# Optimization experiments

Hardware: AMD Instinct MI355X
Metric: run time of the kernel (lower is better)

## Reference

```python
import jax, jax.numpy as jnp
import numpy as np

HEADS = 8
DIM_HEAD = 64
SCALE = 10.0
EPS = 1e-12  # F.normalize eps


def setup_inputs() -> dict:
    key = jax.random.key(0)
    k1, k2, k3, k4 = jax.random.split(key, 4)
    dim, hidden = 256, HEADS * DIM_HEAD
    x = jax.random.normal(k1, (8, dim, 32, 32), dtype=jnp.float32)
    w_qkv = jax.random.normal(k2, (3 * hidden, dim), dtype=jnp.float32) * (1.0 / np.sqrt(dim))
    w_out = jax.random.normal(k3, (dim, hidden), dtype=jnp.float32) * (1.0 / np.sqrt(hidden))
    b_out = jax.random.normal(k4, (dim,), dtype=jnp.float32) * 0.01
    return {"x": x, "w_qkv": w_qkv, "w_out": w_out, "b_out": b_out}


def _l2norm_last(t):
    # matches F.normalize(t, dim=-1): t / max(||t||_2, eps)
    n = jnp.sqrt(jnp.sum(t * t, axis=-1, keepdims=True))
    return t / jnp.maximum(n, EPS)


def reference(x, w_qkv, w_out, b_out):
    b, c, hh, ww = x.shape
    n = hh * ww
    # 1x1 conv == channel matmul
    qkv = jnp.einsum('bcxy,oc->boxy', x, w_qkv)  # (b, 3*hidden, h, w)
    q, k, v = jnp.split(qkv, 3, axis=1)
    # 'b (h c) x y -> b h c (x y)'
    to_heads = lambda t: t.reshape(b, HEADS, DIM_HEAD, n)
    q, k, v = to_heads(q), to_heads(k), to_heads(v)
    # NOTE: l2norm over the LAST axis = spatial token axis n (faithful to source)
    q = _l2norm_last(q)
    k = _l2norm_last(k)
    sim = jnp.einsum('bhdi,bhdj->bhij', q, k) * SCALE  # (b, h, n, n)
    attn = jax.nn.softmax(sim, axis=-1)
    out = jnp.einsum('bhij,bhdj->bhid', attn, v)  # (b, h, n, d)
    # 'b h (x y) d -> b (h d) x y'
    out = out.transpose(0, 1, 3, 2).reshape(b, HEADS * DIM_HEAD, hh, ww)
    return jnp.einsum('bcxy,oc->boxy', out, w_out) + b_out[None, :, None, None]
```

## Files before the change

kernel.cpp:

```cpp
#include <hip/hip_runtime.h>
#include <math.h>

#define NHEADS 8
#define DHEAD  64
#define HIDDEN 512
#define CIN    256
#define NTOK   1024
#define QK_SCALE 10.0f
#define LOG2E 1.44269504088896f
#define MSHIFT 10.5f
#define MBIAS  (-MSHIFT * LOG2E)

typedef __bf16 bf16x8 __attribute__((ext_vector_type(8)));
typedef float  f32x4  __attribute__((ext_vector_type(4)));
typedef unsigned short u16x8 __attribute__((ext_vector_type(8)));
typedef unsigned short u16x4 __attribute__((ext_vector_type(4)));

__device__ inline unsigned short f2bf(float f) {
    unsigned u = __builtin_bit_cast(unsigned, f);
    u = (u + 0x7FFFu + ((u >> 16) & 1u)) >> 16;
    return (unsigned short)u;
}

__device__ inline bf16x8 cvt8(const float* p) {
    float4 a = *(const float4*)p;
    float4 b = *(const float4*)(p + 4);
    u16x8 t;
    t[0] = f2bf(a.x); t[1] = f2bf(a.y); t[2] = f2bf(a.z); t[3] = f2bf(a.w);
    t[4] = f2bf(b.x); t[5] = f2bf(b.y); t[6] = f2bf(b.z); t[7] = f2bf(b.w);
    return __builtin_bit_cast(bf16x8, t);
}

__global__ __launch_bounds__(256)
void cvt_x_kernel(const float* __restrict__ x, unsigned short* __restrict__ xt) {
    const int b  = blockIdx.z;
    const int c0 = blockIdx.y * 64;
    const int n0 = blockIdx.x * 64;
    const float* src = x + ((size_t)b * CIN + c0) * NTOK + n0;
    unsigned short* dst = xt + ((size_t)b * NTOK + n0) * CIN + c0;

    __shared__ float T[64][65];
    const int t = threadIdx.x;
    {
        const int nq = t & 15, cg = t >> 4;
        #pragma unroll
        for (int rr = 0; rr < 4; ++rr) {
            const int c = cg + rr * 16;
            float4 v = *(const float4*)(src + (size_t)c * NTOK + nq * 4);
            T[c][nq * 4 + 0] = v.x;
            T[c][nq * 4 + 1] = v.y;
            T[c][nq * 4 + 2] = v.z;
            T[c][nq * 4 + 3] = v.w;
        }
    }
    __syncthreads();
    {
        const int n = t >> 2, cq = t & 3;
        alignas(16) unsigned short tmp[16];
        #pragma unroll
        for (int e = 0; e < 16; ++e)
            tmp[e] = f2bf(T[cq * 16 + e][n]);
        *(uint4*)(dst + (size_t)n * CIN + cq * 16)     = *(uint4*)&tmp[0];
        *(uint4*)(dst + (size_t)n * CIN + cq * 16 + 8) = *(uint4*)&tmp[8];
    }
}

__global__ __launch_bounds__(256)
void cvt_w_kernel(const float* __restrict__ wq, const float* __restrict__ wo,
                  unsigned short* __restrict__ wqb, unsigned short* __restrict__ wob) {
    const size_t i = ((size_t)blockIdx.x * 256 + threadIdx.x) * 8;
    if (i < (size_t)1536 * 256) {
        *(bf16x8*)(wqb + i) = cvt8(wq + i);
    } else {
        const size_t j = i - (size_t)1536 * 256;
        *(bf16x8*)(wob + j) = cvt8(wo + j);
    }
}

__global__ __launch_bounds__(256)
void gemm1_kernel(const unsigned short* __restrict__ wqb,
                  const unsigned short* __restrict__ xt,
                  float* __restrict__ qt,
                  unsigned short* __restrict__ vb,
                  float* __restrict__ ss) {
    const int b  = blockIdx.z;
    const int bm = blockIdx.y * 128;
    const int bn = blockIdx.x * 128;
    const int wave = threadIdx.x >> 6, lane = threadIdx.x & 63;
    const int lo = lane & 15, hi = lane >> 4;
    const int wm = bm + (wave >> 1) * 64;
    const int wn = bn + (wave & 1) * 64;

    const unsigned short* Ab = wqb + (size_t)(wm + lo) * CIN + hi * 8;
    const unsigned short* Bb = xt + ((size_t)b * NTOK + wn + lo) * CIN + hi * 8;

    f32x4 acc[4][4];
    #pragma unroll
    for (int mi = 0; mi < 4; ++mi)
        #pragma unroll
        for (int ni = 0; ni < 4; ++ni) acc[mi][ni] = (f32x4){0.f, 0.f, 0.f, 0.f};

    for (int k0 = 0; k0 < CIN; k0 += 32) {
        bf16x8 a[4], bf[4];
        #pragma unroll
        for (int mi = 0; mi < 4; ++mi) a[mi]  = *(const bf16x8*)(Ab + (size_t)mi * 16 * CIN + k0);
        #pragma unroll
        for (int ni = 0; ni < 4; ++ni) bf[ni] = *(const bf16x8*)(Bb + (size_t)ni * 16 * CIN + k0);
        #pragma unroll
        for (int mi = 0; mi < 4; ++mi)
            #pragma unroll
            for (int ni = 0; ni < 4; ++ni)
                acc[mi][ni] = __builtin_amdgcn_mfma_f32_16x16x32_bf16(a[mi], bf[ni], acc[mi][ni], 0, 0, 0);
    }

    __shared__ unsigned short VL[4][32][72];

    if (bm < 1024) {
        const int isK = (wm >= 512) ? 1 : 0;
        const int ch0 = wm & 511;
        const int head = ch0 >> 6;
        float* dst = qt + (((size_t)isK * 64 + b * 8 + head) * NTOK) * DHEAD;
        #pragma unroll
        for (int mi = 0; mi < 4; ++mi) {
            const int d = mi * 16 + hi * 4;
            #pragma unroll
            for (int ni = 0; ni < 4; ++ni) {
                const int n = wn + ni * 16 + lo;
                *(f32x4*)(dst + (size_t)n * DHEAD + d) = acc[mi][ni];
            }
        }
        float p[4][4];
        #pragma unroll
        for (int mi = 0; mi < 4; ++mi)
            #pragma unroll
            for (int r = 0; r < 4; ++r) {
                float s = 0.f;
                #pragma unroll
                for (int ni = 0; ni < 4; ++ni) s += acc[mi][ni][r] * acc[mi][ni][r];
                p[mi][r] = s;
            }
        #pragma unroll
        for (int off = 1; off < 16; off <<= 1)
            #pragma unroll
            for (int mi = 0; mi < 4; ++mi)
                #pragma unroll
                for (int r = 0; r < 4; ++r)
                    p[mi][r] += __shfl_xor(p[mi][r], off, 64);
        if (lo == 0) {
            #pragma unroll
            for (int mi = 0; mi < 4; ++mi)
                #pragma unroll
                for (int r = 0; r < 4; ++r)
                    atomicAdd(&ss[(size_t)b * 1024 + isK * 512 + ch0 + mi * 16 + hi * 4 + r], p[mi][r]);
        }
    } else {
        const int ch0 = wm - 1024;
        #pragma unroll
        for (int half = 0; half < 2; ++half) {
            #pragma unroll
            for (int mm = 0; mm < 2; ++mm) {
                const int mi = half * 2 + mm;
                #pragma unroll
                for (int ni = 0; ni < 4; ++ni)
                    #pragma unroll
                    for (int r = 0; r < 4; ++r)
                        VL[wave][mm * 16 + hi * 4 + r][ni * 16 + lo] = f2bf(acc[mi][ni][r]);
            }
            #pragma unroll
            for (int i = 0; i < 4; ++i) {
                const int flat = i * 64 + lane;
                const int row = flat >> 3, c = flat & 7;
                uint4 v = *(uint4*)&VL[wave][row][c * 8];
                const int ch = ch0 + half * 32 + row;
                *(uint4*)(vb + ((size_t)b * HIDDEN + ch) * NTOK + wn + c * 8) = v;
            }
        }
    }
}

__global__ __launch_bounds__(256)
void scale_cvt_kernel(const float* __restrict__ qt, const float* __restrict__ ss,
                      unsigned short* __restrict__ qs, unsigned short* __restrict__ ks) {
    const size_t idx = ((size_t)blockIdx.x * 256 + threadIdx.x) * 8;
    const size_t half = (size_t)64 * NTOK * DHEAD;
    const int isK = idx >= half;
    const size_t rem = idx - (size_t)isK * half;
    const int bh = (int)(rem >> 16);
    const int d0 = (int)(rem & 63);
    const int b  = bh >> 3;
    const int ch = isK * 512 + (bh & 7) * 64 + d0;
    const float scl = isK ? 1.0f : QK_SCALE;

    const float* ip = qt + idx;
    float4 v0 = *(const float4*)ip;
    float4 v1 = *(const float4*)(ip + 4);
    float4 q0 = *(const float4*)(ss + (size_t)b * 1024 + ch);
    float4 q1 = *(const float4*)(ss + (size_t)b * 1024 + ch + 4);
    float4 s0, s1;
    s0.x = 1.0f / fmaxf(sqrtf(q0.x), 1e-12f); s0.y = 1.0f / fmaxf(sqrtf(q0.y), 1e-12f);
    s0.z = 1.0f / fmaxf(sqrtf(q0.z), 1e-12f); s0.w = 1.0f / fmaxf(sqrtf(q0.w), 1e-12f);
    s1.x = 1.0f / fmaxf(sqrtf(q1.x), 1e-12f); s1.y = 1.0f / fmaxf(sqrtf(q1.y), 1e-12f);
    s1.z = 1.0f / fmaxf(sqrtf(q1.z), 1e-12f); s1.w = 1.0f / fmaxf(sqrtf(q1.w), 1e-12f);
    u16x8 t;
    t[0] = f2bf(v0.x * s0.x * scl); t[1] = f2bf(v0.y * s0.y * scl);
    t[2] = f2bf(v0.z * s0.z * scl); t[3] = f2bf(v0.w * s0.w * scl);
    t[4] = f2bf(v1.x * s1.x * scl); t[5] = f2bf(v1.y * s1.y * scl);
    t[6] = f2bf(v1.z * s1.z * scl); t[7] = f2bf(v1.w * s1.w * scl);
    *(u16x8*)((isK ? ks : qs) + rem) = t;
}

__global__ __launch_bounds__(256)
void attn_mfma_kernel(const unsigned short* __restrict__ qs,
                      const unsigned short* __restrict__ ks,
                      const unsigned short* __restrict__ vb,
                      float* __restrict__ po, float* __restrict__ pml) {
    const int hw = blockIdx.x;
    const int virt = (hw & 7) * 128 + (hw >> 3);
    const int bh = virt >> 4;
    const int sub = virt & 15;
    const int it = sub & 7;
    const int js = sub >> 3;
    const int b = bh >> 3, h = bh & 7;

    const int lane = threadIdx.x & 63;
    const int wave = threadIdx.x >> 6;
    const int lo = lane & 15;
    const int hi = lane >> 4;
    const int iw = it * 128 + wave * 32;

    const unsigned short* qbh = qs + (size_t)bh * NTOK * DHEAD;
    const unsigned short* kbh = ks + (size_t)bh * NTOK * DHEAD;
    const unsigned short* vbh = vb + ((size_t)b * HIDDEN + h * DHEAD) * NTOK;

    __shared__ unsigned short Plds[4][2048];
    __shared__ float Tlds[4][16][68];
    char* pbase = (char*)&Plds[wave][0];

    bf16x8 aQ[2][2];
    #pragma unroll
    for (int f = 0; f < 2; ++f) {
        const unsigned short* qp = qbh + (size_t)(iw + f * 16 + lo) * DHEAD + hi * 8;
        aQ[f][0] = *(const bf16x8*)qp;
        aQ[f][1] = *(const bf16x8*)(qp + 32);
    }

    float lsum[2][4];
    #pragma unroll
    for (int f = 0; f < 2; ++f)
        #pragma unroll
        for (int r = 0; r < 4; ++r) lsum[f][r] = 0.0f;
    f32x4 acc[2][4];
    #pragma unroll
    for (int f = 0; f < 2; ++f)
        #pragma unroll
        for (int ds = 0; ds < 4; ++ds) acc[f][ds] = (f32x4){0.f, 0.f, 0.f, 0.f};

    for (int jt = 0; jt < 8; ++jt) {
        const int j0 = js * 512 + jt * 64;

        bf16x8 bV[4][2];
        #pragma unroll
        for (int ds = 0; ds < 4; ++ds) {
            const unsigned short* vp = vbh + (size_t)(ds * 16 + lo) * NTOK + j0 + hi * 8;
            bV[ds][0] = *(const bf16x8*)vp;
            bV[ds][1] = *(const bf16x8*)(vp + 32);
        }

        bf16x8 bK[4][2];
        #pragma unroll
        for (int jj = 0; jj < 4; ++jj) {
            const unsigned short* kp = kbh + (size_t)(j0 + jj * 16 + lo) * DHEAD + hi * 8;
            bK[jj][0] = *(const bf16x8*)kp;
            bK[jj][1] = *(const bf16x8*)(kp + 32);
        }

        f32x4 s[2][4];
        __builtin_amdgcn_s_setprio(1);
        #pragma unroll
        for (int jj = 0; jj < 4; ++jj)
            #pragma unroll
            for (int f = 0; f < 2; ++f) {
                f32x4 c = (f32x4){0.f, 0.f, 0.f, 0.f};
                c = __builtin_amdgcn_mfma_f32_16x16x32_bf16(aQ[f][0], bK[jj][0], c, 0, 0, 0);
                c = __builtin_amdgcn_mfma_f32_16x16x32_bf16(aQ[f][1], bK[jj][1], c, 0, 0, 0);
                s[f][jj] = c;
            }
        __builtin_amdgcn_s_setprio(0);

        #pragma unroll
        for (int f = 0; f < 2; ++f)
            #pragma unroll
            for (int jj = 0; jj < 4; ++jj)
                #pragma unroll
                for (int r = 0; r < 4; ++r) {
                    const float p = __builtin_amdgcn_exp2f(fmaf(s[f][jj][r], LOG2E, MBIAS));
                    lsum[f][r] += p;
                    const int row = f * 16 + hi * 4 + r;
                    const int byte = (row * 128 + (jj * 16 + lo) * 2) ^ ((row & 7) << 4);
                    *(unsigned short*)(pbase + byte) = f2bf(p);
                }

        bf16x8 aP[2][2];
        #pragma unroll
        for (int f = 0; f < 2; ++f) {
            const int row = f * 16 + lo;
            const int swz = (lo & 7) << 4;
            aP[f][0] = *(const bf16x8*)(pbase + ((row * 128 + hi * 16) ^ swz));
            aP[f][1] = *(const bf16x8*)(pbase + ((row * 128 + 64 + hi * 16) ^ swz));
        }
        __builtin_amdgcn_s_setprio(1);
        #pragma unroll
        for (int ds = 0; ds < 4; ++ds)
            #pragma unroll
            for (int f = 0; f < 2; ++f) {
                acc[f][ds] = __builtin_amdgcn_mfma_f32_16x16x32_bf16(aP[f][0], bV[ds][0], acc[f][ds], 0, 0, 0);
                acc[f][ds] = __builtin_amdgcn_mfma_f32_16x16x32_bf16(aP[f][1], bV[ds][1], acc[f][ds], 0, 0, 0);
            }
        __builtin_amdgcn_s_setprio(0);
    }

    #pragma unroll
    for (int off = 1; off < 16; off <<= 1)
        #pragma unroll
        for (int f = 0; f < 2; ++f)
            #pragma unroll
            for (int r = 0; r < 4; ++r)
                lsum[f][r] += __shfl_xor(lsum[f][r], off, 64);

    float* pob = po + ((size_t)(js * 64 + bh) * NTOK + iw) * DHEAD;
    #pragma unroll
    for (int f = 0; f < 2; ++f) {
        #pragma unroll
        for (int ds = 0; ds < 4; ++ds)
            #pragma unroll
            for (int r = 0; r < 4; ++r)
                Tlds[wave][hi * 4 + r][ds * 16 + lo] = acc[f][ds][r];
        #pragma unroll
        for (int pass = 0; pass < 4; ++pass) {
            const int flat = pass * 64 + lane;
            const int row = flat >> 4, dq = flat & 15;
            float4 v = *(float4*)&Tlds[wave][row][dq * 4];
            *(float4*)(pob + (size_t)(f * 16 + row) * DHEAD + dq * 4) = v;
        }
        if (lo == 0) {
            #pragma unroll
            for (int r = 0; r < 4; ++r) {
                const int row = iw + f * 16 + hi * 4 + r;
                pml[(size_t)(js * 64 + bh) * NTOK + row] = lsum[f][r];
            }
        }
    }
}

__global__ __launch_bounds__(256)
void combine_kernel(const float* __restrict__ po, const float* __restrict__ pml,
                    unsigned short* __restrict__ attn_t) {
    const size_t fl = ((size_t)blockIdx.x * 256 + threadIdx.x) * 4;
    const int bh  = (int)(fl >> 16);
    const int rem = (int)(fl & 65535);
    const int row = rem >> 6;
    const int d   = rem & 63;
    const int b = bh >> 3, h = bh & 7;
    const size_t SS = (size_t)64 * NTOK * DHEAD;

    const float l1 = pml[(size_t)bh * NTOK + row];
    const float l2 = pml[(size_t)(64 + bh) * NTOK + row];
    const float inv = 1.0f / (l1 + l2);

    const float4 o1 = *(const float4*)(po + fl);
    const float4 o2 = *(const float4*)(po + SS + fl);
    u16x4 r;
    r[0] = f2bf((o1.x + o2.x) * inv);
    r[1] = f2bf((o1.y + o2.y) * inv);
    r[2] = f2bf((o1.z + o2.z) * inv);
    r[3] = f2bf((o1.w + o2.w) * inv);
    *(u16x4*)(attn_t + ((size_t)b * NTOK + row) * HIDDEN + h * DHEAD + d) = r;
}

__global__ __launch_bounds__(128)
void gemm2_kernel(const unsigned short* __restrict__ wob,
                  const unsigned short* __restrict__ attn_t,
                  const float* __restrict__ b_out,
                  float* __restrict__ out) {
    const int b  = blockIdx.z;
    const int bm = blockIdx.y * 64;
    const int bn = blockIdx.x * 128;
    const int wave = threadIdx.x >> 6, lane = threadIdx.x & 63;
    const int lo = lane & 15, hi = lane >> 4;
    const int wn = bn + wave * 64;

    const unsigned short* Ab = wob + (size_t)(bm + lo) * HIDDEN + hi * 8;
    const unsigned short* Bb = attn_t + ((size_t)b * NTOK + wn + lo) * HIDDEN + hi * 8;

    f32x4 acc[4][4];
    #pragma unroll
    for (int mi = 0; mi < 4; ++mi)
        #pragma unroll
        for (int ni = 0; ni < 4; ++ni) acc[mi][ni] = (f32x4){0.f, 0.f, 0.f, 0.f};

    for (int k0 = 0; k0 < HIDDEN; k0 += 32) {
        bf16x8 a[4], bf[4];
        #pragma unroll
        for (int mi = 0; mi < 4; ++mi) a[mi]  = *(const bf16x8*)(Ab + (size_t)mi * 16 * HIDDEN + k0);
        #pragma unroll
        for (int ni = 0; ni < 4; ++ni) bf[ni] = *(const bf16x8*)(Bb + (size_t)ni * 16 * HIDDEN + k0);
        #pragma unroll
        for (int mi = 0; mi < 4; ++mi)
            #pragma unroll
            for (int ni = 0; ni < 4; ++ni)
                acc[mi][ni] = __builtin_amdgcn_mfma_f32_16x16x32_bf16(a[mi], bf[ni], acc[mi][ni], 0, 0, 0);
    }

    __shared__ float OL[2][32][69];
    #pragma unroll
    for (int half = 0; half < 2; ++half) {
        #pragma unroll
        for (int mm = 0; mm < 2; ++mm) {
            const int mi = half * 2 + mm;
            #pragma unroll
            for (int ni = 0; ni < 4; ++ni)
                #pragma unroll
                for (int r = 0; r < 4; ++r)
                    OL[wave][mm * 16 + hi * 4 + r][ni * 16 + lo] = acc[mi][ni][r];
        }
        #pragma unroll
        for (int i = 0; i < 8; ++i) {
            const int flat = i * 64 + lane;
            const int row = flat >> 4, c = flat & 15;
            float4 v = *(float4*)&OL[wave][row][c * 4];
            const int m = bm + half * 32 + row;
            const float bb = b_out[m];
            v.x += bb; v.y += bb; v.z += bb; v.w += bb;
            *(float4*)(out + ((size_t)b * CIN + m) * NTOK + wn + c * 4) = v;
        }
    }
}

extern "C" void kernel_launch(void* const* d_in, const int* in_sizes, int n_in,
                              void* d_out, int out_size, void* d_ws, size_t ws_size,
                              hipStream_t stream) {
    const float* x     = (const float*)d_in[0];
    const float* w_qkv = (const float*)d_in[1];
    const float* w_out = (const float*)d_in[2];
    const float* b_out = (const float*)d_in[3];
    float* out = (float*)d_out;

    char* ws = (char*)d_ws;
    unsigned short* xt  = (unsigned short*)(ws);
    unsigned short* wqb = (unsigned short*)(ws + 4194304);
    unsigned short* wob = (unsigned short*)(ws + 4980736);
    float*          ss  = (float*)(ws + 5242880);
    unsigned short* qs  = (unsigned short*)(ws + 5308416);
    unsigned short* ks  = (unsigned short*)(ws + 13697024);
    unsigned short* vb  = (unsigned short*)(ws + 22085632);
    float*          qt  = (float*)(ws + 30474240);
    float*          po  = (float*)(ws + 30474240);
    unsigned short* attn_t = (unsigned short*)(ws + 5308416);
    float*          pml = (float*)(ws + 64028672);

    hipMemsetAsync(ss, 0, 8 * 1024 * sizeof(float), stream);

    cvt_x_kernel<<<dim3(16, 4, 8), 256, 0, stream>>>(x, xt);
    cvt_w_kernel<<<256, 256, 0, stream>>>(w_qkv, w_out, wqb, wob);

    gemm1_kernel<<<dim3(8, 12, 8), 256, 0, stream>>>(wqb, xt, qt, vb, ss);

    scale_cvt_kernel<<<4096, 256, 0, stream>>>(qt, ss, qs, ks);

    attn_mfma_kernel<<<1024, 256, 0, stream>>>(qs, ks, vb, po, pml);

    combine_kernel<<<4096, 256, 0, stream>>>(po, pml, attn_t);

    gemm2_kernel<<<dim3(8, 4, 8), 128, 0, stream>>>(wob, attn_t, b_out, out);
}
```

Measured before the change: 203.1 us.

## Keep softmax probabilities in registers via transposed MFMA, store partials as bf16

Swaps the operand order of the QK^T MFMA so the score tile comes out laid out to be reused directly as the B operand of the PV MFMA. V is loaded in matching 4-element chunks, and the probabilities are packed with v_cvt_pk_bf16_f32, which removes the LDS round trip for P. The partial output buffer becomes bf16 and the LDS transpose before the output store is dropped, which halves partial-output traffic read by the combine kernel. Blocks shrink to 2 waves with twice the grid. Storing partials in bf16 costs some accuracy before the final normalisation.

```diff
diff --git a/kernel.cpp b/kernel.cpp
--- a/kernel.cpp
+++ b/kernel.cpp
@@ -12,7 +12,9 @@
 #define MBIAS  (-MSHIFT * LOG2E)
 
 typedef __bf16 bf16x8 __attribute__((ext_vector_type(8)));
+typedef __bf16 bf16x4 __attribute__((ext_vector_type(4)));
 typedef float  f32x4  __attribute__((ext_vector_type(4)));
+typedef unsigned u32x4 __attribute__((ext_vector_type(4)));
 typedef unsigned short u16x8 __attribute__((ext_vector_type(8)));
 typedef unsigned short u16x4 __attribute__((ext_vector_type(4)));
 
@@ -20,6 +22,16 @@
     unsigned u = __builtin_bit_cast(unsigned, f);
     u = (u + 0x7FFFu + ((u >> 16) & 1u)) >> 16;
     return (unsigned short)u;
+}
+
+__device__ inline unsigned cvtpk(float a, float b) {
+    unsigned w;
+    asm("v_cvt_pk_bf16_f32 %0, %1, %2" : "=v"(w) : "v"(a), "v"(b));
+    return w;
+}
+
+__device__ inline float bf2f(unsigned short u) {
+    return __builtin_bit_cast(float, (unsigned)u << 16);
 }
 
 __device__ inline bf16x8 cvt8(const float* p) {
@@ -209,32 +221,28 @@
     *(u16x8*)((isK ? ks : qs) + rem) = t;
 }
 
-__global__ __launch_bounds__(256)
+__global__ __launch_bounds__(128)
 void attn_mfma_kernel(const unsigned short* __restrict__ qs,
                       const unsigned short* __restrict__ ks,
                       const unsigned short* __restrict__ vb,
-                      float* __restrict__ po, float* __restrict__ pml) {
+                      unsigned short* __restrict__ po, float* __restrict__ pml) {
     const int hw = blockIdx.x;
-    const int virt = (hw & 7) * 128 + (hw >> 3);
-    const int bh = virt >> 4;
-    const int sub = virt & 15;
-    const int it = sub & 7;
-    const int js = sub >> 3;
+    const int virt = (hw & 7) * 256 + (hw >> 3);
+    const int bh  = virt >> 5;
+    const int sub = virt & 31;
+    const int it  = sub & 15;
+    const int js  = sub >> 4;
     const int b = bh >> 3, h = bh & 7;
 
     const int lane = threadIdx.x & 63;
     const int wave = threadIdx.x >> 6;
     const int lo = lane & 15;
     const int hi = lane >> 4;
-    const int iw = it * 128 + wave * 32;
+    const int iw = it * 64 + wave * 32;
 
     const unsigned short* qbh = qs + (size_t)bh * NTOK * DHEAD;
     const unsigned short* kbh = ks + (size_t)bh * NTOK * DHEAD;
     const unsigned short* vbh = vb + ((size_t)b * HIDDEN + h * DHEAD) * NTOK;
-
-    __shared__ unsigned short Plds[4][2048];
-    __shared__ float Tlds[4][16][68];
-    char* pbase = (char*)&Plds[wave][0];
 
     bf16x8 aQ[2][2];
     #pragma unroll
@@ -244,11 +252,7 @@
         aQ[f][1] = *(const bf16x8*)(qp + 32);
     }
 
-    float lsum[2][4];
-    #pragma unroll
-    for (int f = 0; f < 2; ++f)
-        #pragma unroll
-        for (int r = 0; r < 4; ++r) lsum[f][r] = 0.0f;
+    float lsum[2] = {0.0f, 0.0f};
     f32x4 acc[2][4];
     #pragma unroll
     for (int f = 0; f < 2; ++f)
@@ -258,12 +262,13 @@
     for (int jt = 0; jt < 8; ++jt) {
         const int j0 = js * 512 + jt * 64;
 
-        bf16x8 bV[4][2];
+        bf16x4 bV[4][4];
         #pragma unroll
         for (int ds = 0; ds < 4; ++ds) {
-            const unsigned short* vp = vbh + (size_t)(ds * 16 + lo) * NTOK + j0 + hi * 8;
-            bV[ds][0] = *(const bf16x8*)vp;
-            bV[ds][1] = *(const bf16x8*)(vp + 32);
+            const unsigned short* vp = vbh + (size_t)(ds * 16 + lo) * NTOK + j0 + hi * 4;
+            #pragma unroll
+            for (int u = 0; u < 4; ++u)
+                bV[ds][u] = *(const bf16x4*)(vp + u * 16);
         }
 
         bf16x8 bK[4][2];
@@ -281,79 +286,71 @@
             #pragma unroll
             for (int f = 0; f < 2; ++f) {
                 f32x4 c = (f32x4){0.f, 0.f, 0.f, 0.f};
-                c = __builtin_amdgcn_mfma_f32_16x16x32_bf16(aQ[f][0], bK[jj][0], c, 0, 0, 0);
-                c = __builtin_amdgcn_mfma_f32_16x16x32_bf16(aQ[f][1], bK[jj][1], c, 0, 0, 0);
+                c = __builtin_amdgcn_mfma_f32_16x16x32_bf16(bK[jj][0], aQ[f][0], c, 0, 0, 0);
+                c = __builtin_amdgcn_mfma_f32_16x16x32_bf16(bK[jj][1], aQ[f][1], c, 0, 0, 0);
                 s[f][jj] = c;
             }
         __builtin_amdgcn_s_setprio(0);
 
-        #pragma unroll
-        for (int f = 0; f < 2; ++f)
+        unsigned pw[2][2][4];
+        #pragma unroll
+        for (int f = 0; f < 2; ++f) {
             #pragma unroll
             for (int jj = 0; jj < 4; ++jj)
                 #pragma unroll
                 for (int r = 0; r < 4; ++r) {
                     const float p = __builtin_amdgcn_exp2f(fmaf(s[f][jj][r], LOG2E, MBIAS));
-                    lsum[f][r] += p;
-                    const int row = f * 16 + hi * 4 + r;
-                    const int byte = (row * 128 + (jj * 16 + lo) * 2) ^ ((row & 7) << 4);
-                    *(unsigned short*)(pbase + byte) = f2bf(p);
+                    s[f][jj][r] = p;
+                    lsum[f] += p;
                 }
-
-        bf16x8 aP[2][2];
-        #pragma unroll
-        for (int f = 0; f < 2; ++f) {
-            const int row = f * 16 + lo;
-            const int swz = (lo & 7) << 4;
-            aP[f][0] = *(const bf16x8*)(pbase + ((row * 128 + hi * 16) ^ swz));
-            aP[f][1] = *(const bf16x8*)(pbase + ((row * 128 + 64 + hi * 16) ^ swz));
-        }
+            #pragma unroll
+            for (int t = 0; t < 2; ++t) {
+                pw[f][t][0] = cvtpk(s[f][2 * t][0],     s[f][2 * t][1]);
+                pw[f][t][1] = cvtpk(s[f][2 * t][2],     s[f][2 * t][3]);
+                pw[f][t][2] = cvtpk(s[f][2 * t + 1][0], s[f][2 * t + 1][1]);
+                pw[f][t][3] = cvtpk(s[f][2 * t + 1][2], s[f][2 * t + 1][3]);
+            }
+        }
+
         __builtin_amdgcn_s_setprio(1);
         #pragma unroll
         for (int ds = 0; ds < 4; ++ds)
             #pragma unroll
-            for (int f = 0; f < 2; ++f) {
-                acc[f][ds] = __builtin_amdgcn_mfma_f32_16x16x32_bf16(aP[f][0], bV[ds][0], acc[f][ds], 0, 0, 0);
-                acc[f][ds] = __builtin_amdgcn_mfma_f32_16x16x32_bf16(aP[f][1], bV[ds][1], acc[f][ds], 0, 0, 0);
-            }
+            for (int f = 0; f < 2; ++f)
+                #pragma unroll
+                for (int t = 0; t < 2; ++t) {
+                    const bf16x8 av = __builtin_shufflevector(
+                        bV[ds][2 * t], bV[ds][2 * t + 1], 0, 1, 2, 3, 4, 5, 6, 7);
+                    const bf16x8 bp = __builtin_bit_cast(bf16x8,
+                        (u32x4){pw[f][t][0], pw[f][t][1], pw[f][t][2], pw[f][t][3]});
+                    acc[f][ds] = __builtin_amdgcn_mfma_f32_16x16x32_bf16(av, bp, acc[f][ds], 0, 0, 0);
+                }
         __builtin_amdgcn_s_setprio(0);
     }
 
     #pragma unroll
-    for (int off = 1; off < 16; off <<= 1)
-        #pragma unroll
-        for (int f = 0; f < 2; ++f)
-            #pragma unroll
-            for (int r = 0; r < 4; ++r)
-                lsum[f][r] += __shfl_xor(lsum[f][r], off, 64);
-
-    float* pob = po + ((size_t)(js * 64 + bh) * NTOK + iw) * DHEAD;
-    #pragma unroll
     for (int f = 0; f < 2; ++f) {
-        #pragma unroll
-        for (int ds = 0; ds < 4; ++ds)
-            #pragma unroll
-            for (int r = 0; r < 4; ++r)
-                Tlds[wave][hi * 4 + r][ds * 16 + lo] = acc[f][ds][r];
-        #pragma unroll
-        for (int pass = 0; pass < 4; ++pass) {
-            const int flat = pass * 64 + lane;
-            const int row = flat >> 4, dq = flat & 15;
-            float4 v = *(float4*)&Tlds[wave][row][dq * 4];
-            *(float4*)(pob + (size_t)(f * 16 + row) * DHEAD + dq * 4) = v;
-        }
-        if (lo == 0) {
-            #pragma unroll
-            for (int r = 0; r < 4; ++r) {
-                const int row = iw + f * 16 + hi * 4 + r;
-                pml[(size_t)(js * 64 + bh) * NTOK + row] = lsum[f][r];
-            }
-        }
+        lsum[f] += __shfl_xor(lsum[f], 16, 64);
+        lsum[f] += __shfl_xor(lsum[f], 32, 64);
+    }
+
+    unsigned short* pob = po + ((size_t)(js * 64 + bh) * NTOK + iw) * DHEAD;
+    #pragma unroll
+    for (int f = 0; f < 2; ++f) {
+        #pragma unroll
+        for (int ds = 0; ds < 4; ++ds) {
+            uint2 w;
+            w.x = cvtpk(acc[f][ds][0], acc[f][ds][1]);
+            w.y = cvtpk(acc[f][ds][2], acc[f][ds][3]);
+            *(uint2*)(pob + (size_t)(f * 16 + lo) * DHEAD + ds * 16 + hi * 4) = w;
+        }
+        if (hi == 0)
+            pml[(size_t)(js * 64 + bh) * NTOK + iw + f * 16 + lo] = lsum[f];
     }
 }
 
 __global__ __launch_bounds__(256)
-void combine_kernel(const float* __restrict__ po, const float* __restrict__ pml,
+void combine_kernel(const unsigned short* __restrict__ po, const float* __restrict__ pml,
                     unsigned short* __restrict__ attn_t) {
     const size_t fl = ((size_t)blockIdx.x * 256 + threadIdx.x) * 4;
     const int bh  = (int)(fl >> 16);
@@ -367,13 +364,12 @@
     const float l2 = pml[(size_t)(64 + bh) * NTOK + row];
     const float inv = 1.0f / (l1 + l2);
 
-    const float4 o1 = *(const float4*)(po + fl);
-    const float4 o2 = *(const float4*)(po + SS + fl);
+    const u16x4 o1 = *(const u16x4*)(po + fl);
+    const u16x4 o2 = *(const u16x4*)(po + SS + fl);
     u16x4 r;
-    r[0] = f2bf((o1.x + o2.x) * inv);
-    r[1] = f2bf((o1.y + o2.y) * inv);
-    r[2] = f2bf((o1.z + o2.z) * inv);
-    r[3] = f2bf((o1.w + o2.w) * inv);
+    #pragma unroll
+    for (int e = 0; e < 4; ++e)
+        r[e] = f2bf((bf2f(o1[e]) + bf2f(o2[e])) * inv);
     *(u16x4*)(attn_t + ((size_t)b * NTOK + row) * HIDDEN + h * DHEAD + d) = r;
 }
 
@@ -454,7 +450,7 @@
     unsigned short* ks  = (unsigned short*)(ws + 13697024);
     unsigned short* vb  = (unsigned short*)(ws + 22085632);
     float*          qt  = (float*)(ws + 30474240);
-    float*          po  = (float*)(ws + 30474240);
+    unsigned short* po  = (unsigned short*)(ws + 30474240);
     unsigned short* attn_t = (unsigned short*)(ws + 5308416);
     float*          pml = (float*)(ws + 64028672);
 
@@ -467,7 +463,7 @@
 
     scale_cvt_kernel<<<4096, 256, 0, stream>>>(qt, ss, qs, ks);
 
-    attn_mfma_kernel<<<1024, 256, 0, stream>>>(qs, ks, vb, po, pml);
+    attn_mfma_kernel<<<2048, 128, 0, stream>>>(qs, ks, vb, po, pml);
 
     combine_kernel<<<4096, 256, 0, stream>>>(po, pml, attn_t);
 
```

Measured after the change: 229.1 us. +12.8%, slower.
